# Kernel optimization log

Measured on AMD Instinct MI355X. Metric: run time of the kernel, lower is better.

Reference implementation:

```python
import jax, jax.numpy as jnp
import numpy as np

B, T, D = 256, 256, 96   # batch, seq (== block_size), d_model
H, E = 6, 16             # n_head, d_head = d_model // n_head
DFF = 4 * D              # feedforward hidden = 384
NOISE_STD = 0.1
EPS = 1e-5               # torch LayerNorm default eps


def setup_inputs() -> dict:
    key = jax.random.key(0)
    ks = jax.random.split(key, 10)
    s = 0.02
    return {
        "x":     jax.random.normal(ks[0], (B, T, D), jnp.float32),
        # per-head Q/K/V projections stacked: [H, D, E] (no bias, as in Head)
        "Wq":    jax.random.normal(ks[1], (H, D, E), jnp.float32) * s,
        "Wk":    jax.random.normal(ks[2], (H, D, E), jnp.float32) * s,
        "Wv":    jax.random.normal(ks[3], (H, D, E), jnp.float32) * s,
        "Wp":    jax.random.normal(ks[4], (D, D), jnp.float32) * s,
        "bp":    jnp.zeros((D,), jnp.float32),
        "ln1_g": jnp.ones((D,), jnp.float32),
        "ln1_b": jnp.zeros((D,), jnp.float32),
        "ln2_g": jnp.ones((D,), jnp.float32),
        "ln2_b": jnp.zeros((D,), jnp.float32),
        "W1":    jax.random.normal(ks[5], (D, DFF), jnp.float32) * s,
        "b1":    jnp.zeros((DFF,), jnp.float32),
        "W2":    jax.random.normal(ks[6], (DFF, D), jnp.float32) * s,
        "b2":    jnp.zeros((D,), jnp.float32),
    }


def layernorm(x, g, b):
    m = jnp.mean(x, axis=-1, keepdims=True)
    v = jnp.var(x, axis=-1, keepdims=True)
    return (x - m) * jax.lax.rsqrt(v + EPS) * g + b


def reference(x, Wq, Wk, Wv, Wp, bp, ln1_g, ln1_b, ln2_g, ln2_b, W1, b1, W2, b2):
    Bx, Tx, Dx = x.shape
    nk1, nk2 = jax.random.split(jax.random.key(42), 2)

    # --- self-attention branch (pre-norm) ---
    h = layernorm(x, ln1_g, ln1_b)
    q = jnp.einsum('btd,hde->bhte', h, Wq)
    k = jnp.einsum('btd,hde->bhte', h, Wk)
    v = jnp.einsum('btd,hde->bhte', h, Wv)
    scores = jnp.einsum('bhte,bhse->bhts', q, k) * (E ** -0.5)
    causal = jnp.tril(jnp.ones((Tx, Tx), bool))
    scores = jnp.where(causal, scores, -jnp.inf)
    a = jax.nn.softmax(scores, axis=-1)      # dropout = identity (eval)
    o = jnp.einsum('bhts,bhse->bhte', a, v)
    o = o.transpose(0, 2, 1, 3).reshape(Bx, Tx, Dx)  # concat heads
    o = o @ Wp + bp
    x = x + o + jax.random.normal(nk1, x.shape, x.dtype) * NOISE_STD

    # --- feedforward branch (pre-norm) ---
    h = layernorm(x, ln2_g, ln2_b)
    f = jax.nn.relu(h @ W1 + b1) @ W2 + b2   # dropout = identity (eval)
    x = x + f + jax.random.normal(nk2, x.shape, x.dtype) * NOISE_STD
    return x
```

## Files before the change

### kernel.cpp

```cpp
#include <hip/hip_runtime.h>
#include <hip/hip_bf16.h>
#include <stdint.h>


#define B_    256
#define T_    256
#define D_    96
#define H_    6
#define E_    16
#define DFF_  384
#define BT_   (B_*T_)
#define NTOK_ (BT_*D_)
#define WPN_  (96*96)
#define W1N_  (96*384)
#define W2N_  (384*96)
#define WTOT_ (WPN_+W1N_+W2N_)

typedef __hip_bfloat16 bf16;
typedef __attribute__((ext_vector_type(8))) short v8s;
typedef __attribute__((ext_vector_type(4))) float v4f;

__host__ __device__ inline uint32_t rotl32(uint32_t x, int r){ return (x<<r)|(x>>(32-r)); }

__host__ __device__ inline void tf2x32(uint32_t k0, uint32_t k1, uint32_t& x0, uint32_t& x1){
  uint32_t ks2 = k0 ^ k1 ^ 0x1BD11BDAu;
  x0 += k0; x1 += k1;
#define TF_R(r) { x0 += x1; x1 = rotl32(x1, r); x1 ^= x0; }
  TF_R(13) TF_R(15) TF_R(26) TF_R(6)
  x0 += k1;  x1 += ks2 + 1u;
  TF_R(17) TF_R(29) TF_R(16) TF_R(24)
  x0 += ks2; x1 += k0 + 2u;
  TF_R(13) TF_R(15) TF_R(26) TF_R(6)
  x0 += k0;  x1 += k1 + 3u;
  TF_R(17) TF_R(29) TF_R(16) TF_R(24)
  x0 += k1;  x1 += ks2 + 4u;
  TF_R(13) TF_R(15) TF_R(26) TF_R(6)
  x0 += ks2; x1 += k0 + 5u;
#undef TF_R
}

__device__ __forceinline__ float erfinv32(float x){
  float w = -0.69314718056f * __log2f((1.0f - x) * (1.0f + x));
  float p;
  if (w < 5.0f) {
    w -= 2.5f;
    p = 2.81022636e-08f;
    p = fmaf(p, w, 3.43273939e-07f);
    p = fmaf(p, w, -3.5233877e-06f);
    p = fmaf(p, w, -4.39150654e-06f);
    p = fmaf(p, w, 0.00021858087f);
    p = fmaf(p, w, -0.00125372503f);
    p = fmaf(p, w, -0.00417768164f);
    p = fmaf(p, w, 0.246640727f);
    p = fmaf(p, w, 1.50140941f);
  } else {
    w = sqrtf(w) - 3.0f;
    p = -0.000200214257f;
    p = fmaf(p, w, 0.000100950558f);
    p = fmaf(p, w, 0.00134934322f);
    p = fmaf(p, w, -0.00367342844f);
    p = fmaf(p, w, 0.00573950773f);
    p = fmaf(p, w, -0.0076224613f);
    p = fmaf(p, w, 0.00943887047f);
    p = fmaf(p, w, 1.00167406f);
    p = fmaf(p, w, 2.83297682f);
  }
  return p * x;
}

__device__ __forceinline__ float jax_normal(uint32_t k0, uint32_t k1, uint32_t j){
  uint32_t x0 = 0u, x1 = j;
  tf2x32(k0, k1, x0, x1);
  uint32_t bits = x0 ^ x1;
  float f = __uint_as_float((bits >> 9) | 0x3F800000u) - 1.0f;
  const float lo = -0.99999994f;
  float u = fmaxf(lo, fmaf(f, 2.0f, lo));
  return 1.41421356f * erfinv32(u);
}

__device__ __forceinline__ float blo(uint32_t u){ return __uint_as_float(u << 16); }
__device__ __forceinline__ float bhi(uint32_t u){ return __uint_as_float(u & 0xFFFF0000u); }
__device__ __forceinline__ uint16_t f2b(float f){
  union { bf16 h; uint16_t u; } x; x.h = __float2bfloat16(f); return x.u;
}
__device__ __forceinline__ uint32_t packbf(float a, float b){
  return (uint32_t)f2b(a) | ((uint32_t)f2b(b) << 16);
}

__global__ __launch_bounds__(256)
void k_prep(const float* __restrict__ Wp, const float* __restrict__ W1,
            const float* __restrict__ W2, bf16* __restrict__ wb)
{
  int id = blockIdx.x*256 + threadIdx.x;
  const float* src; bf16* dst; int k, n, N;
  if (id < WPN_)               { src = Wp; dst = wb;              k = id/96;  n = id%96;  N = 96;  }
  else if (id < WPN_ + W1N_)   { int t = id - WPN_;
                                 src = W1; dst = wb + WPN_;        k = t/384;  n = t%384;  N = 384; }
  else                         { int t = id - WPN_ - W1N_;
                                 src = W2; dst = wb + WPN_ + W1N_; k = t/96;   n = t%96;   N = 96;  }
  int idx = ((k>>3)*(N>>4) + (n>>4))*128 + ((n&15)<<3) + (k&7);
  dst[idx] = __float2bfloat16(src[(size_t)k*N + n]);
}

__global__ __launch_bounds__(256)
void k_attn_fused(const float* __restrict__ x,
                  const float* __restrict__ Wq, const float* __restrict__ Wk,
                  const float* __restrict__ Wv,
                  const float* __restrict__ g1, const float* __restrict__ bln1,
                  bf16* __restrict__ o_ws)
{
  __shared__ __align__(16) uint16_t hts[64][104];
  __shared__ __align__(16) uint32_t wpl[48][52];
  __shared__ __align__(16) uint16_t Qs[256][40];
  __shared__ __align__(16) uint16_t Ks[256][40];
  __shared__ __align__(16) uint16_t Vt[16][264];
  __shared__ __align__(16) uint16_t Pb[4][16][40];

  const int tid  = threadIdx.x;
  const int bh   = blockIdx.x;
  const int b    = bh / H_, h = bh % H_;
  const int w    = tid >> 6;
  const int lane = tid & 63;
  const int quad = lane >> 4;
  const int l15  = lane & 15;

  for (int idx = tid; idx < 48*48; idx += 256) {
    int c = idx / 48, dp = idx % 48;
    int mat = c >> 4, e = c & 15;
    const float* Wm = (mat == 0 ? Wk : (mat == 1 ? Wv : Wq)) + h*(D_*E_);
    wpl[c][dp] = packbf(Wm[(2*dp)*16 + e], Wm[(2*dp+1)*16 + e]);
  }
  for (int i = tid; i < 4096; i += 256) {
    int row = i >> 4, c = 16 + (i & 15);
    Qs[row][c] = 0; Ks[row][c] = 0;
  }

  {
    const int r  = tid >> 2;
    const int cg = tid & 3;
    float gv[24], bv[24];
    #pragma unroll
    for (int i = 0; i < 24; ++i) { gv[i] = g1[cg*24 + i]; bv[i] = bln1[cg*24 + i]; }

    for (int rt = 0; rt < 4; ++rt) {
      __syncthreads();
      const int row = rt*64 + r;
      const float4* xp = (const float4*)(x + ((size_t)(b*256 + row)*96 + cg*24));
      float xv[24];
      #pragma unroll
      for (int p = 0; p < 6; ++p) {
        float4 t4 = xp[p];
        xv[4*p+0] = t4.x; xv[4*p+1] = t4.y; xv[4*p+2] = t4.z; xv[4*p+3] = t4.w;
      }
      float s1 = 0.f, s2 = 0.f;
      #pragma unroll
      for (int i = 0; i < 24; ++i) { s1 += xv[i]; s2 = fmaf(xv[i], xv[i], s2); }
      s1 += __shfl_xor(s1, 1); s2 += __shfl_xor(s2, 1);
      s1 += __shfl_xor(s1, 2); s2 += __shfl_xor(s2, 2);
      float mm = s1 * (1.0f/96.0f);
      float rs = rsqrtf(s2 * (1.0f/96.0f) - mm*mm + 1e-5f);
      #pragma unroll
      for (int p = 0; p < 12; ++p) {
        float h0 = (xv[2*p]   - mm)*rs*gv[2*p]   + bv[2*p];
        float h1 = (xv[2*p+1] - mm)*rs*gv[2*p+1] + bv[2*p+1];
        *(uint32_t*)&hts[r][cg*24 + 2*p] = packbf(h0, h1);
      }
      __syncthreads();

      v8s ah[3];
      #pragma unroll
      for (int ks = 0; ks < 3; ++ks)
        ah[ks] = *(const v8s*)&hts[w*16 + l15][ks*32 + quad*8];
      #pragma unroll
      for (int nt = 0; nt < 3; ++nt) {
        v4f acc = {0.f,0.f,0.f,0.f};
        #pragma unroll
        for (int ks = 0; ks < 3; ++ks) {
          v8s bb = *(const v8s*)&wpl[nt*16 + l15][ks*16 + quad*4];
          acc = __builtin_amdgcn_mfma_f32_16x16x32_bf16(ah[ks], bb, acc, 0, 0, 0);
        }
        int tr0 = rt*64 + w*16 + quad*4;
        if (nt == 0) {
          #pragma unroll
          for (int r2 = 0; r2 < 4; ++r2) Ks[tr0 + r2][l15] = f2b(acc[r2]);
        } else if (nt == 1) {
          *(uint32_t*)&Vt[l15][tr0]     = packbf(acc[0], acc[1]);
          *(uint32_t*)&Vt[l15][tr0 + 2] = packbf(acc[2], acc[3]);
        } else {
          #pragma unroll
          for (int r2 = 0; r2 < 4; ++r2) Qs[tr0 + r2][l15] = f2b(acc[r2] * 0.25f);
        }
      }
    }
  }
  __syncthreads();

  v8s ones;
  #pragma unroll
  for (int j = 0; j < 8; ++j) ones[j] = (short)0x3F80;

  v8s qf[4];
  v4f oacc[4], lac[4];
  #pragma unroll
  for (int i = 0; i < 4; ++i) {
    int mt = w + 4*i;
    qf[i] = *(const v8s*)&Qs[mt*16 + l15][quad*8];
    oacc[i] = (v4f){0.f,0.f,0.f,0.f};
    lac[i]  = (v4f){0.f,0.f,0.f,0.f};
  }

  for (int sb = 0; sb < 8; ++sb) {
    v8s kf0 = *(const v8s*)&Ks[sb*32      + l15][quad*8];
    v8s kf1 = *(const v8s*)&Ks[sb*32 + 16 + l15][quad*8];
    v8s vf  = *(const v8s*)&Vt[l15][sb*32 + quad*8];
    #pragma unroll
    for (int i = 0; i < 4; ++i) {
      int mt = w + 4*i;
      if (mt >= 2*sb) {
        v4f z = {0.f,0.f,0.f,0.f};
        v4f s0 = __builtin_amdgcn_mfma_f32_16x16x32_bf16(qf[i], kf0, z, 0, 0, 0);
        v4f s1 = __builtin_amdgcn_mfma_f32_16x16x32_bf16(qf[i], kf1, z, 0, 0, 0);
        const int qb  = mt*16 + quad*4;
        const int sc0 = sb*32 + l15, sc1 = sc0 + 16;
        #pragma unroll
        for (int r2 = 0; r2 < 4; ++r2) {
          float p0 = (sc0 > qb + r2) ? 0.f : __expf(s0[r2]);
          float p1 = (sc1 > qb + r2) ? 0.f : __expf(s1[r2]);
          Pb[w][quad*4 + r2][l15]      = f2b(p0);
          Pb[w][quad*4 + r2][16 + l15] = f2b(p1);
        }
        v8s pf = *(const v8s*)&Pb[w][l15][quad*8];
        oacc[i] = __builtin_amdgcn_mfma_f32_16x16x32_bf16(pf, vf,   oacc[i], 0, 0, 0);
        lac[i]  = __builtin_amdgcn_mfma_f32_16x16x32_bf16(pf, ones, lac[i],  0, 0, 0);
      }
    }
  }

  #pragma unroll
  for (int i = 0; i < 4; ++i) {
    int mt = w + 4*i;
    #pragma unroll
    for (int r2 = 0; r2 < 4; ++r2) {
      float inv = 1.0f / lac[i][r2];
      size_t idx = ((size_t)b*256 + mt*16 + quad*4 + r2)*96 + h*16 + l15;
      o_ws[idx] = __float2bfloat16(oacc[i][r2] * inv);
    }
  }
}

__global__ __launch_bounds__(256, 4)
void k_proj_ff(const float* __restrict__ x, const bf16* __restrict__ o_ws,
               const bf16* __restrict__ wb,
               const float* __restrict__ bp,
               const float* __restrict__ g2, const float* __restrict__ bln2,
               const float* __restrict__ b1, const float* __restrict__ b2,
               float* __restrict__ out,
               uint32_t n1k0, uint32_t n1k1, uint32_t n2k0, uint32_t n2k1)
{
  __shared__ __align__(16) uint8_t smem[13312 + 26624];
  uint16_t (*x1t)[104] = (uint16_t(*)[104])&smem[0];
  uint16_t (*h2t)[104] = (uint16_t(*)[104])&smem[13312];
  uint16_t (*f1t)[104] = (uint16_t(*)[104])&smem[26624];
  float*    cs         = (float*)&smem[13312];

  const bf16* wpb = wb;
  const bf16* w1b = wb + WPN_;
  const bf16* w2b = wb + WPN_ + W1N_;

  const int tid  = threadIdx.x;
  const int w    = tid >> 6;
  const int lane = tid & 63;
  const int quad = lane >> 4;
  const int l15  = lane & 15;
  const int rowbase = blockIdx.x * 64;
  const uint32_t jbase = (uint32_t)rowbase * 96u;

  #define BFRAG(Wb, Ndiv16, nt, k8) \
    (*(const v8s*)((Wb) + (((k8)*(Ndiv16) + (nt))*128 + l15*8)))

  {
    v8s ao[3];
    #pragma unroll
    for (int ks = 0; ks < 3; ++ks)
      ao[ks] = *(const v8s*)(o_ws + (size_t)(rowbase + w*16 + l15)*96 + ks*32 + quad*8);
    #pragma unroll
    for (int nt = 0; nt < 6; ++nt) {
      int col = nt*16 + l15;
      v4f acc = {0.f,0.f,0.f,0.f};
      #pragma unroll
      for (int ks = 0; ks < 3; ++ks)
        acc = __builtin_amdgcn_mfma_f32_16x16x32_bf16(ao[ks], BFRAG(wpb, 6, nt, ks*4+quad), acc, 0, 0, 0);
      float bpv = bp[col];
      #pragma unroll
      for (int r = 0; r < 4; ++r) {
        int row = w*16 + quad*4 + r;
        uint32_t j = jbase + (uint32_t)row*96u + (uint32_t)col;
        x1t[row][col] = f2b(acc[r] + bpv + x[j] + 0.1f * jax_normal(n1k0, n1k1, j));
      }
    }
  }

  {
    int row = tid >> 2, cg = tid & 3;
    const uint32_t* xr = (const uint32_t*)&x1t[row][cg*24];
    float v[24];
    #pragma unroll
    for (int p = 0; p < 12; ++p) { uint32_t u = xr[p]; v[2*p] = blo(u); v[2*p+1] = bhi(u); }
    float s1 = 0.f, s2 = 0.f;
    #pragma unroll
    for (int i = 0; i < 24; ++i) { s1 += v[i]; s2 = fmaf(v[i], v[i], s2); }
    s1 += __shfl_xor(s1, 1); s2 += __shfl_xor(s2, 1);
    s1 += __shfl_xor(s1, 2); s2 += __shfl_xor(s2, 2);
    float mm = s1 * (1.0f/96.0f);
    float rs = rsqrtf(s2 * (1.0f/96.0f) - mm*mm + 1e-5f);
    uint32_t* hw = (uint32_t*)&h2t[row][cg*24];
    #pragma unroll
    for (int p = 0; p < 12; ++p) {
      int c = cg*24 + 2*p;
      float h0 = (v[2*p]   - mm)*rs*g2[c]   + bln2[c];
      float h1 = (v[2*p+1] - mm)*rs*g2[c+1] + bln2[c+1];
      hw[p] = packbf(h0, h1);
    }
  }

  v8s ah[3];
  #pragma unroll
  for (int ks = 0; ks < 3; ++ks)
    ah[ks] = *(const v8s*)&h2t[w*16 + l15][ks*32 + quad*8];
  v4f acc2[6];
  #pragma unroll
  for (int nt = 0; nt < 6; ++nt) acc2[nt] = (v4f){0.f,0.f,0.f,0.f};

  for (int c = 0; c < 4; ++c) {
    #pragma unroll
    for (int nt = 0; nt < 6; ++nt) {
      v4f a = {0.f,0.f,0.f,0.f};
      #pragma unroll
      for (int ks = 0; ks < 3; ++ks)
        a = __builtin_amdgcn_mfma_f32_16x16x32_bf16(ah[ks], BFRAG(w1b, 24, c*6+nt, ks*4+quad), a, 0, 0, 0);
      float b1v = b1[c*96 + nt*16 + l15];
      #pragma unroll
      for (int r = 0; r < 4; ++r)
        f1t[w*16 + quad*4 + r][nt*16 + l15] = f2b(fmaxf(a[r] + b1v, 0.f));
    }
    v8s af[3];
    #pragma unroll
    for (int ks = 0; ks < 3; ++ks)
      af[ks] = *(const v8s*)&f1t[w*16 + l15][ks*32 + quad*8];
    #pragma unroll
    for (int nt = 0; nt < 6; ++nt) {
      #pragma unroll
      for (int ks = 0; ks < 3; ++ks)
        acc2[nt] = __builtin_amdgcn_mfma_f32_16x16x32_bf16(af[ks], BFRAG(w2b, 6, nt, (c*3+ks)*4+quad), acc2[nt], 0, 0, 0);
    }
  }

  __syncthreads();
  #pragma unroll
  for (int nt = 0; nt < 6; ++nt) {
    int col = nt*16 + l15;
    #pragma unroll
    for (int r = 0; r < 4; ++r)
      cs[(w*16 + quad*4 + r)*97 + col] = acc2[nt][r];
  }
  __syncthreads();

  float* outp = out + (size_t)rowbase*96;
  for (int i = tid; i < 6144; i += 256) {
    int row = i / 96, col = i % 96;
    float x1v = blo((uint32_t)x1t[row][col]);
    outp[i] = x1v + cs[row*97 + col] + b2[col]
            + 0.1f * jax_normal(n2k0, n2k1, jbase + (uint32_t)i);
  }
  #undef BFRAG
}

__global__ __launch_bounds__(256)
void k_zero(float* __restrict__ out)
{
  int i = blockIdx.x*256 + threadIdx.x;
  if (i < NTOK_) out[i] = 0.0f;
}

extern "C" void kernel_launch(void* const* d_in, const int* in_sizes, int n_in,
                              void* d_out, int out_size, void* d_ws, size_t ws_size,
                              hipStream_t stream) {
  const float* x    = (const float*)d_in[0];
  const float* Wq   = (const float*)d_in[1];
  const float* Wk   = (const float*)d_in[2];
  const float* Wv   = (const float*)d_in[3];
  const float* Wp   = (const float*)d_in[4];
  const float* bp   = (const float*)d_in[5];
  const float* g1   = (const float*)d_in[6];
  const float* bln1 = (const float*)d_in[7];
  const float* g2   = (const float*)d_in[8];
  const float* bln2 = (const float*)d_in[9];
  const float* W1   = (const float*)d_in[10];
  const float* b1   = (const float*)d_in[11];
  const float* W2   = (const float*)d_in[12];
  const float* b2   = (const float*)d_in[13];
  float* out = (float*)d_out;

  size_t need = (size_t)NTOK_*sizeof(bf16) + (size_t)WTOT_*sizeof(bf16);
  if (ws_size < need) {
    hipLaunchKernelGGL(k_zero, dim3((NTOK_ + 255)/256), dim3(256), 0, stream, out);
    return;
  }
  bf16* o_ws = (bf16*)d_ws;
  bf16* wbuf = o_ws + NTOK_;

  uint32_t n1k0 = 0u, n1k1 = 0u; tf2x32(0u, 42u, n1k0, n1k1);
  uint32_t n2k0 = 0u, n2k1 = 1u; tf2x32(0u, 42u, n2k0, n2k1);

  hipLaunchKernelGGL(k_prep, dim3(WTOT_/256), dim3(256), 0, stream,
                     Wp, W1, W2, wbuf);
  hipLaunchKernelGGL(k_attn_fused, dim3(B_*H_), dim3(256), 0, stream,
                     x, Wq, Wk, Wv, g1, bln1, o_ws);
  hipLaunchKernelGGL(k_proj_ff, dim3(BT_/64), dim3(256), 0, stream,
                     x, o_ws, wbuf, bp, g2, bln2, b1, b2, out,
                     n1k0, n1k1, n2k0, n2k1);
}
```

Measured before the change: 226.9 us.

## Fold weight prep into attention kernel and shrink LDS with wave-local buffers

Removes the separate weight-conversion launch by having each attention block convert 54 weight elements. Shrinks LDS in both kernels: Q is kept in registers and staged through a wave-private slice of the LayerNorm buffer, K is stored unpadded with zeroed upper fragments, and the FF kernel reuses one buffer for the LayerNorm output and the hidden activations. Block-wide barriers become compiler-only fences because each wave now touches only its own rows, and the final output is written straight from accumulators instead of going through an LDS staging tile. These changes aim at more blocks per CU (launch bounds 256,3) and less sync overhead, but they rely on wave-lockstep LDS visibility without real barriers, and the direct output stores are less coalesced.

```diff
diff --git a/kernel.cpp b/kernel.cpp
--- a/kernel.cpp
+++ b/kernel.cpp
@@ -19,6 +19,8 @@
 typedef __hip_bfloat16 bf16;
 typedef __attribute__((ext_vector_type(8))) short v8s;
 typedef __attribute__((ext_vector_type(4))) float v4f;
+
+__device__ __forceinline__ void wfence(){ __asm__ volatile("" ::: "memory"); }
 
 __host__ __device__ inline uint32_t rotl32(uint32_t x, int r){ return (x<<r)|(x>>(32-r)); }
 
@@ -87,34 +89,19 @@
   return (uint32_t)f2b(a) | ((uint32_t)f2b(b) << 16);
 }
 
-__global__ __launch_bounds__(256)
-void k_prep(const float* __restrict__ Wp, const float* __restrict__ W1,
-            const float* __restrict__ W2, bf16* __restrict__ wb)
-{
-  int id = blockIdx.x*256 + threadIdx.x;
-  const float* src; bf16* dst; int k, n, N;
-  if (id < WPN_)               { src = Wp; dst = wb;              k = id/96;  n = id%96;  N = 96;  }
-  else if (id < WPN_ + W1N_)   { int t = id - WPN_;
-                                 src = W1; dst = wb + WPN_;        k = t/384;  n = t%384;  N = 384; }
-  else                         { int t = id - WPN_ - W1N_;
-                                 src = W2; dst = wb + WPN_ + W1N_; k = t/96;   n = t%96;   N = 96;  }
-  int idx = ((k>>3)*(N>>4) + (n>>4))*128 + ((n&15)<<3) + (k&7);
-  dst[idx] = __float2bfloat16(src[(size_t)k*N + n]);
-}
-
-__global__ __launch_bounds__(256)
+__global__ __launch_bounds__(256, 3)
 void k_attn_fused(const float* __restrict__ x,
                   const float* __restrict__ Wq, const float* __restrict__ Wk,
                   const float* __restrict__ Wv,
                   const float* __restrict__ g1, const float* __restrict__ bln1,
-                  bf16* __restrict__ o_ws)
+                  bf16* __restrict__ o_ws,
+                  const float* __restrict__ Wp, const float* __restrict__ W1,
+                  const float* __restrict__ W2, bf16* __restrict__ wbuf)
 {
-  __shared__ __align__(16) uint16_t hts[64][104];
+  __shared__ __align__(16) uint16_t hts[64*104];
   __shared__ __align__(16) uint32_t wpl[48][52];
-  __shared__ __align__(16) uint16_t Qs[256][40];
-  __shared__ __align__(16) uint16_t Ks[256][40];
+  __shared__ __align__(16) uint16_t Ks[256][24];
   __shared__ __align__(16) uint16_t Vt[16][264];
-  __shared__ __align__(16) uint16_t Pb[4][16][40];
 
   const int tid  = threadIdx.x;
   const int bh   = blockIdx.x;
@@ -124,27 +111,37 @@
   const int quad = lane >> 4;
   const int l15  = lane & 15;
 
+  if (tid < 54) {
+    int id = bh*54 + tid;
+    const float* src; bf16* dst; int k, n, N;
+    if (id < WPN_)             { src = Wp; dst = wbuf;               k = id/96; n = id%96; N = 96; }
+    else if (id < WPN_ + W1N_) { int t = id - WPN_;
+                                 src = W1; dst = wbuf + WPN_;        k = t/384; n = t%384; N = 384; }
+    else                       { int t = id - WPN_ - W1N_;
+                                 src = W2; dst = wbuf + WPN_ + W1N_; k = t/96;  n = t%96;  N = 96; }
+    int idx = ((k>>3)*(N>>4) + (n>>4))*128 + ((n&15)<<3) + (k&7);
+    dst[idx] = __float2bfloat16(src[(size_t)k*N + n]);
+  }
+
   for (int idx = tid; idx < 48*48; idx += 256) {
     int c = idx / 48, dp = idx % 48;
     int mat = c >> 4, e = c & 15;
     const float* Wm = (mat == 0 ? Wk : (mat == 1 ? Wv : Wq)) + h*(D_*E_);
     wpl[c][dp] = packbf(Wm[(2*dp)*16 + e], Wm[(2*dp+1)*16 + e]);
   }
-  for (int i = tid; i < 4096; i += 256) {
-    int row = i >> 4, c = 16 + (i & 15);
-    Qs[row][c] = 0; Ks[row][c] = 0;
-  }
-
+
+  v4f qacc[4];
   {
-    const int r  = tid >> 2;
-    const int cg = tid & 3;
+    const int r  = lane >> 2;
+    const int cg = lane & 3;
     float gv[24], bv[24];
     #pragma unroll
     for (int i = 0; i < 24; ++i) { gv[i] = g1[cg*24 + i]; bv[i] = bln1[cg*24 + i]; }
 
     for (int rt = 0; rt < 4; ++rt) {
       __syncthreads();
-      const int row = rt*64 + r;
+      const int lrow = w*16 + r;
+      const int row  = rt*64 + lrow;
       const float4* xp = (const float4*)(x + ((size_t)(b*256 + row)*96 + cg*24));
       float xv[24];
       #pragma unroll
@@ -163,14 +160,14 @@
       for (int p = 0; p < 12; ++p) {
         float h0 = (xv[2*p]   - mm)*rs*gv[2*p]   + bv[2*p];
         float h1 = (xv[2*p+1] - mm)*rs*gv[2*p+1] + bv[2*p+1];
-        *(uint32_t*)&hts[r][cg*24 + 2*p] = packbf(h0, h1);
+        *(uint32_t*)&hts[lrow*104 + cg*24 + 2*p] = packbf(h0, h1);
       }
       __syncthreads();
 
       v8s ah[3];
       #pragma unroll
       for (int ks = 0; ks < 3; ++ks)
-        ah[ks] = *(const v8s*)&hts[w*16 + l15][ks*32 + quad*8];
+        ah[ks] = *(const v8s*)&hts[(w*16 + l15)*104 + ks*32 + quad*8];
       #pragma unroll
       for (int nt = 0; nt < 3; ++nt) {
         v4f acc = {0.f,0.f,0.f,0.f};
@@ -187,49 +184,59 @@
           *(uint32_t*)&Vt[l15][tr0]     = packbf(acc[0], acc[1]);
           *(uint32_t*)&Vt[l15][tr0 + 2] = packbf(acc[2], acc[3]);
         } else {
-          #pragma unroll
-          for (int r2 = 0; r2 < 4; ++r2) Qs[tr0 + r2][l15] = f2b(acc[r2] * 0.25f);
+          qacc[rt] = acc;
         }
       }
     }
   }
   __syncthreads();
 
+  uint16_t* Pb = &hts[(w*16)*104];
+  v8s qf[4];
+  v8s zero8;
+  #pragma unroll
+  for (int j = 0; j < 8; ++j) zero8[j] = 0;
+  #pragma unroll
+  for (int rt = 0; rt < 4; ++rt) {
+    wfence();
+    #pragma unroll
+    for (int r2 = 0; r2 < 4; ++r2)
+      Pb[(quad*4 + r2)*40 + l15] = f2b(qacc[rt][r2] * 0.25f);
+    wfence();
+    qf[rt] = (quad < 2) ? *(const v8s*)&Pb[l15*40 + quad*8] : zero8;
+  }
+
   v8s ones;
   #pragma unroll
   for (int j = 0; j < 8; ++j) ones[j] = (short)0x3F80;
 
-  v8s qf[4];
   v4f oacc[4], lac[4];
   #pragma unroll
-  for (int i = 0; i < 4; ++i) {
-    int mt = w + 4*i;
-    qf[i] = *(const v8s*)&Qs[mt*16 + l15][quad*8];
-    oacc[i] = (v4f){0.f,0.f,0.f,0.f};
-    lac[i]  = (v4f){0.f,0.f,0.f,0.f};
-  }
+  for (int i = 0; i < 4; ++i) { oacc[i] = (v4f){0.f,0.f,0.f,0.f}; lac[i] = (v4f){0.f,0.f,0.f,0.f}; }
 
   for (int sb = 0; sb < 8; ++sb) {
-    v8s kf0 = *(const v8s*)&Ks[sb*32      + l15][quad*8];
-    v8s kf1 = *(const v8s*)&Ks[sb*32 + 16 + l15][quad*8];
+    v8s kf0 = (quad < 2) ? *(const v8s*)&Ks[sb*32      + l15][quad*8] : zero8;
+    v8s kf1 = (quad < 2) ? *(const v8s*)&Ks[sb*32 + 16 + l15][quad*8] : zero8;
     v8s vf  = *(const v8s*)&Vt[l15][sb*32 + quad*8];
     #pragma unroll
     for (int i = 0; i < 4; ++i) {
-      int mt = w + 4*i;
+      int mt = 4*i + w;
       if (mt >= 2*sb) {
         v4f z = {0.f,0.f,0.f,0.f};
         v4f s0 = __builtin_amdgcn_mfma_f32_16x16x32_bf16(qf[i], kf0, z, 0, 0, 0);
         v4f s1 = __builtin_amdgcn_mfma_f32_16x16x32_bf16(qf[i], kf1, z, 0, 0, 0);
         const int qb  = mt*16 + quad*4;
         const int sc0 = sb*32 + l15, sc1 = sc0 + 16;
+        wfence();
         #pragma unroll
         for (int r2 = 0; r2 < 4; ++r2) {
           float p0 = (sc0 > qb + r2) ? 0.f : __expf(s0[r2]);
           float p1 = (sc1 > qb + r2) ? 0.f : __expf(s1[r2]);
-          Pb[w][quad*4 + r2][l15]      = f2b(p0);
-          Pb[w][quad*4 + r2][16 + l15] = f2b(p1);
+          Pb[(quad*4 + r2)*40 + l15]      = f2b(p0);
+          Pb[(quad*4 + r2)*40 + 16 + l15] = f2b(p1);
         }
-        v8s pf = *(const v8s*)&Pb[w][l15][quad*8];
+        wfence();
+        v8s pf = *(const v8s*)&Pb[l15*40 + quad*8];
         oacc[i] = __builtin_amdgcn_mfma_f32_16x16x32_bf16(pf, vf,   oacc[i], 0, 0, 0);
         lac[i]  = __builtin_amdgcn_mfma_f32_16x16x32_bf16(pf, ones, lac[i],  0, 0, 0);
       }
@@ -238,7 +245,7 @@
 
   #pragma unroll
   for (int i = 0; i < 4; ++i) {
-    int mt = w + 4*i;
+    int mt = 4*i + w;
     #pragma unroll
     for (int r2 = 0; r2 < 4; ++r2) {
       float inv = 1.0f / lac[i][r2];
@@ -257,11 +264,8 @@
                float* __restrict__ out,
                uint32_t n1k0, uint32_t n1k1, uint32_t n2k0, uint32_t n2k1)
 {
-  __shared__ __align__(16) uint8_t smem[13312 + 26624];
-  uint16_t (*x1t)[104] = (uint16_t(*)[104])&smem[0];
-  uint16_t (*h2t)[104] = (uint16_t(*)[104])&smem[13312];
-  uint16_t (*f1t)[104] = (uint16_t(*)[104])&smem[26624];
-  float*    cs         = (float*)&smem[13312];
+  __shared__ __align__(16) uint16_t x1t[64][104];
+  __shared__ __align__(16) uint16_t t2 [64][104];
 
   const bf16* wpb = wb;
   const bf16* w1b = wb + WPN_;
@@ -299,9 +303,10 @@
       }
     }
   }
+  wfence();
 
   {
-    int row = tid >> 2, cg = tid & 3;
+    int row = w*16 + (lane >> 2), cg = lane & 3;
     const uint32_t* xr = (const uint32_t*)&x1t[row][cg*24];
     float v[24];
     #pragma unroll
@@ -313,7 +318,7 @@
     s1 += __shfl_xor(s1, 2); s2 += __shfl_xor(s2, 2);
     float mm = s1 * (1.0f/96.0f);
     float rs = rsqrtf(s2 * (1.0f/96.0f) - mm*mm + 1e-5f);
-    uint32_t* hw = (uint32_t*)&h2t[row][cg*24];
+    uint32_t* hw = (uint32_t*)&t2[row][cg*24];
     #pragma unroll
     for (int p = 0; p < 12; ++p) {
       int c = cg*24 + 2*p;
@@ -322,16 +327,18 @@
       hw[p] = packbf(h0, h1);
     }
   }
+  wfence();
 
   v8s ah[3];
   #pragma unroll
   for (int ks = 0; ks < 3; ++ks)
-    ah[ks] = *(const v8s*)&h2t[w*16 + l15][ks*32 + quad*8];
+    ah[ks] = *(const v8s*)&t2[w*16 + l15][ks*32 + quad*8];
   v4f acc2[6];
   #pragma unroll
   for (int nt = 0; nt < 6; ++nt) acc2[nt] = (v4f){0.f,0.f,0.f,0.f};
 
   for (int c = 0; c < 4; ++c) {
+    wfence();
     #pragma unroll
     for (int nt = 0; nt < 6; ++nt) {
       v4f a = {0.f,0.f,0.f,0.f};
@@ -341,12 +348,13 @@
       float b1v = b1[c*96 + nt*16 + l15];
       #pragma unroll
       for (int r = 0; r < 4; ++r)
-        f1t[w*16 + quad*4 + r][nt*16 + l15] = f2b(fmaxf(a[r] + b1v, 0.f));
-    }
+        t2[w*16 + quad*4 + r][nt*16 + l15] = f2b(fmaxf(a[r] + b1v, 0.f));
+    }
+    wfence();
     v8s af[3];
     #pragma unroll
     for (int ks = 0; ks < 3; ++ks)
-      af[ks] = *(const v8s*)&f1t[w*16 + l15][ks*32 + quad*8];
+      af[ks] = *(const v8s*)&t2[w*16 + l15][ks*32 + quad*8];
     #pragma unroll
     for (int nt = 0; nt < 6; ++nt) {
       #pragma unroll
@@ -354,23 +362,20 @@
         acc2[nt] = __builtin_amdgcn_mfma_f32_16x16x32_bf16(af[ks], BFRAG(w2b, 6, nt, (c*3+ks)*4+quad), acc2[nt], 0, 0, 0);
     }
   }
-
-  __syncthreads();
+  wfence();
+
   #pragma unroll
   for (int nt = 0; nt < 6; ++nt) {
     int col = nt*16 + l15;
-    #pragma unroll
-    for (int r = 0; r < 4; ++r)
-      cs[(w*16 + quad*4 + r)*97 + col] = acc2[nt][r];
-  }
-  __syncthreads();
-
-  float* outp = out + (size_t)rowbase*96;
-  for (int i = tid; i < 6144; i += 256) {
-    int row = i / 96, col = i % 96;
-    float x1v = blo((uint32_t)x1t[row][col]);
-    outp[i] = x1v + cs[row*97 + col] + b2[col]
-            + 0.1f * jax_normal(n2k0, n2k1, jbase + (uint32_t)i);
+    float b2v = b2[col];
+    #pragma unroll
+    for (int r = 0; r < 4; ++r) {
+      int row = w*16 + quad*4 + r;
+      uint32_t j = jbase + (uint32_t)row*96u + (uint32_t)col;
+      float x1v = blo((uint32_t)x1t[row][col]);
+      out[(size_t)rowbase*96 + (size_t)row*96 + col] =
+          x1v + acc2[nt][r] + b2v + 0.1f * jax_normal(n2k0, n2k1, j);
+    }
   }
   #undef BFRAG
 }
@@ -412,10 +417,8 @@
   uint32_t n1k0 = 0u, n1k1 = 0u; tf2x32(0u, 42u, n1k0, n1k1);
   uint32_t n2k0 = 0u, n2k1 = 1u; tf2x32(0u, 42u, n2k0, n2k1);
 
-  hipLaunchKernelGGL(k_prep, dim3(WTOT_/256), dim3(256), 0, stream,
-                     Wp, W1, W2, wbuf);
   hipLaunchKernelGGL(k_attn_fused, dim3(B_*H_), dim3(256), 0, stream,
-                     x, Wq, Wk, Wv, g1, bln1, o_ws);
+                     x, Wq, Wk, Wv, g1, bln1, o_ws, Wp, W1, W2, wbuf);
   hipLaunchKernelGGL(k_proj_ff, dim3(BT_/64), dim3(256), 0, stream,
                      x, o_ws, wbuf, bp, g2, bln2, b1, b2, out,
                      n1k0, n1k1, n2k0, n2k1);
```

After: 211.2 us. -6.9%, faster.
